# Performance work log

Hardware: AMD Instinct MI355X
Metric: run time of the kernel (lower is better)

The kernel has to match this reference:

```python
import jax, jax.numpy as jnp
import numpy as np

RC = 6.0            # cosine cutoff radius (Angstrom)
N_ANGULAR = 128     # module init arg; output dim = 3*N_ANGULAR
EPS = 1e-12


def cosine_cutoff(d):
    # Behler-style cosine cutoff: 0.5*(cos(pi*d/rc)+1) for d < rc, else 0
    return jnp.where(d < RC, 0.5 * (jnp.cos(jnp.pi * d / RC) + 1.0), 0.0)


def setup_inputs() -> dict:
    key = jax.random.key(0)
    k1, k2, k3, k4 = jax.random.split(key, 4)
    B, N, M = 8, 4096, 96
    L = 20.0  # box length
    positions = jax.random.uniform(k1, (B, N, 3), dtype=jnp.float32) * L
    cell = jnp.tile(jnp.eye(3, dtype=jnp.float32) * L, (B, 1, 1))
    neighbors = jax.random.randint(k2, (B, N, M), 0, N, dtype=jnp.int32)
    offsets = jax.random.randint(k3, (B, N, M, 3), -1, 2).astype(jnp.float32)
    mask = (jax.random.uniform(k4, (B, N, M)) > 0.1).astype(jnp.float32)
    return {"positions": positions, "cell": cell, "offsets": offsets,
            "mask": mask, "neighbors": neighbors}


def reference(positions, cell, offsets, mask, neighbors):
    B, N, M = neighbors.shape
    # gather neighbor positions: pos_j[b,n,m,:] = positions[b, neighbors[b,n,m], :]
    idx = neighbors.reshape(B, N * M)
    pos_j = jnp.take_along_axis(positions, idx[:, :, None], axis=1).reshape(B, N, M, 3)
    # displacement vectors with periodic offsets (offsets in cell coordinates)
    dis_vec = pos_j - positions[:, :, None, :] + jnp.einsum('bnmi,bij->bnmj', offsets, cell)
    distances = jnp.sqrt(jnp.sum(dis_vec * dis_vec, axis=-1) + EPS)  # [B,N,M]
    # cutoff / distance, zeroed where mask == 0
    cut = jnp.where(mask != 0.0, cosine_cutoff(distances) / distances, 0.0)
    # sort neighbors by descending cut value, gather cut-weighted vectors in that order
    order = jnp.argsort(-cut, axis=-1)                       # [B,N,M]
    cut_vec = cut[..., None] * dis_vec                       # [B,N,M,3]
    cut_vec = jnp.take_along_axis(cut_vec, order[..., None], axis=2)
    cut_vec = cut_vec.reshape(B, N, M * 3)
    # scatter into zero-padded descriptor of width 3*n_angular
    f = jnp.zeros((B, N, N_ANGULAR * 3), dtype=positions.dtype)
    f = f.at[:, :, : M * 3].set(cut_vec)
    return f
```

## Files before the change

kernel.cpp:

```cpp
#include <hip/hip_runtime.h>
#include <math.h>

#define M_NB   96
#define OUT_W  384
#define NATOM  4096
#define WPB    16
#define NITER  4

struct Pst {
    int    jA, jB;
    float  mkA, mkB;
    float3 oA, oB;
};

struct Gth {
    float4 pi, pjA, pjB;
};

__device__ __forceinline__ void load_pst(Pst& s,
    const int* __restrict__ nb, const float* __restrict__ mk,
    const float* __restrict__ of, long q, int lane, bool low)
{
    const long eA = q * M_NB + lane;
    s.jA  = nb[eA];
    s.mkA = mk[eA];
    s.oA  = *(const float3*)(of + eA * 3);
    if (low) {
        const long eB = eA + 64;
        s.jB  = nb[eB];
        s.mkB = mk[eB];
        s.oB  = *(const float3*)(of + eB * 3);
    } else {
        s.jB = 0; s.mkB = 0.f; s.oB = make_float3(0.f, 0.f, 0.f);
    }
}

__device__ __forceinline__ void merge3(float4& a4, float2& a2, int base,
                                       float v0, float v1, float v2, int lane)
{
    const int f4lo = 4 * lane;
    const int f2lo = 256 + 2 * lane;
    const float v[3] = {v0, v1, v2};
    #pragma unroll
    for (int t = 0; t < 3; ++t) {
        const int idx = base + t;
        if      (idx == f4lo)     a4.x = v[t];
        else if (idx == f4lo + 1) a4.y = v[t];
        else if (idx == f4lo + 2) a4.z = v[t];
        else if (idx == f4lo + 3) a4.w = v[t];
        else if (idx == f2lo)     a2.x = v[t];
        else if (idx == f2lo + 1) a2.y = v[t];
    }
}

__global__ __launch_bounds__(64 * WPB, 8) void deepmd_angular_kernel(
    const float* __restrict__ positions,
    const float* __restrict__ cell,
    const float* __restrict__ offsets,
    const float* __restrict__ mask,
    const int*   __restrict__ neighbors,
    float*       __restrict__ out,
    int N)
{
    __shared__ float4 pos4_s[NATOM];

    const int tid  = threadIdx.x;
    const int wv   = tid >> 6;
    const int lane = tid & 63;
    const bool low = lane < 32;

    const int p0 = blockIdx.x * (WPB * NITER);
    const int b  = p0 / N;

    {
        const float* pb_ = positions + (size_t)b * N * 3;
        for (int a = tid; a < NATOM; a += 64 * WPB) {
            const float3 v = *(const float3*)(pb_ + 3 * a);
            pos4_s[a] = make_float4(v.x, v.y, v.z, 0.f);
        }
    }
    __syncthreads();

    const float* cb = cell + (size_t)b * 9;
    const float c00 = cb[0], c01 = cb[1], c02 = cb[2];
    const float c10 = cb[3], c11 = cb[4], c12 = cb[5];
    const float c20 = cb[6], c21 = cb[7], c22 = cb[8];

    const long qb = (long)(p0 + wv * NITER);

    Pst s0, s1;
    load_pst(s0, neighbors, mask, offsets, qb + 0, lane, low);
    load_pst(s1, neighbors, mask, offsets, qb + 1, lane, low);
    Gth g0;
    g0.pi  = pos4_s[(int)(qb + 0) - b * N];
    g0.pjA = pos4_s[s0.jA];
    g0.pjB = pos4_s[s0.jB];

    #pragma unroll
    for (int it = 0; it < NITER; ++it) {
        Pst nxs;
        if (it + 2 < NITER)
            load_pst(nxs, neighbors, mask, offsets, qb + it + 2, lane, low);
        Gth g1;
        if (it + 1 < NITER) {
            g1.pi  = pos4_s[(int)(qb + it + 1) - b * N];
            g1.pjA = pos4_s[s1.jA];
            g1.pjB = pos4_s[s1.jB];
        }

        const int q = (int)qb + it;

        const float dxA = g0.pjA.x - g0.pi.x + s0.oA.x * c00 + s0.oA.y * c10 + s0.oA.z * c20;
        const float dyA = g0.pjA.y - g0.pi.y + s0.oA.x * c01 + s0.oA.y * c11 + s0.oA.z * c21;
        const float dzA = g0.pjA.z - g0.pi.z + s0.oA.x * c02 + s0.oA.y * c12 + s0.oA.z * c22;
        const float dA  = sqrtf(dxA * dxA + dyA * dyA + dzA * dzA + 1e-12f);
        float cutA = 0.f;
        if (s0.mkA != 0.f && dA < 6.f)
            cutA = 0.5f * (__cosf(dA * 0.52359877559829887f) + 1.f) / dA;

        float dxB = 0.f, dyB = 0.f, dzB = 0.f, cutB = 0.f;
        if (low) {
            dxB = g0.pjB.x - g0.pi.x + s0.oB.x * c00 + s0.oB.y * c10 + s0.oB.z * c20;
            dyB = g0.pjB.y - g0.pi.y + s0.oB.x * c01 + s0.oB.y * c11 + s0.oB.z * c21;
            dzB = g0.pjB.z - g0.pi.z + s0.oB.x * c02 + s0.oB.y * c12 + s0.oB.z * c22;
            const float dB = sqrtf(dxB * dxB + dyB * dyB + dzB * dzB + 1e-12f);
            if (s0.mkB != 0.f && dB < 6.f)
                cutB = 0.5f * (__cosf(dB * 0.52359877559829887f) + 1.f) / dB;
        }

        const float w0A = cutA * dxA, w1A = cutA * dyA, w2A = cutA * dzA;
        const float w0B = cutB * dxB, w1B = cutB * dyB, w2B = cutB * dzB;

        float4 a4 = make_float4(0.f, 0.f, 0.f, 0.f);
        float2 a2 = make_float2(0.f, 0.f);

        unsigned long long t = __ballot(cutA != 0.f);
        while (t) {
            const int s = (int)__builtin_ctzll(t); t &= t - 1;
            const float c = __shfl(cutA, s);
            const unsigned long long gtA = __ballot(cutA > c);
            const unsigned long long gtB = __ballot(cutB > c);
            const unsigned long long eqA = __ballot(cutA == c);
            const int rank = __popcll(gtA) + __popcll(gtB)
                           + __popcll(eqA & ((1ull << s) - 1ull));
            merge3(a4, a2, 3 * rank,
                   __shfl(w0A, s), __shfl(w1A, s), __shfl(w2A, s), lane);
        }
        t = __ballot(cutB != 0.f);
        while (t) {
            const int s = (int)__builtin_ctzll(t); t &= t - 1;
            const float c = __shfl(cutB, s);
            const unsigned long long gtA = __ballot(cutA > c);
            const unsigned long long gtB = __ballot(cutB > c);
            const unsigned long long eqA = __ballot(cutA == c);
            const unsigned long long eqB = __ballot(cutB == c);
            const int rank = __popcll(gtA) + __popcll(gtB) + __popcll(eqA)
                           + __popcll(eqB & ((1ull << s) - 1ull));
            merge3(a4, a2, 3 * rank,
                   __shfl(w0B, s), __shfl(w1B, s), __shfl(w2B, s), lane);
        }

        float* rowp = out + (size_t)q * OUT_W;
        ((float4*)rowp)[lane] = a4;
        ((float2*)(rowp + 256))[lane] = a2;

        s0 = s1; s1 = nxs; g0 = g1;
    }
}

extern "C" void kernel_launch(void* const* d_in, const int* in_sizes, int n_in,
                              void* d_out, int out_size, void* d_ws, size_t ws_size,
                              hipStream_t stream) {
    const float* positions = (const float*)d_in[0];
    const float* cell      = (const float*)d_in[1];
    const float* offsets   = (const float*)d_in[2];
    const float* mask      = (const float*)d_in[3];
    const int*   neighbors = (const int*)d_in[4];
    float*       out       = (float*)d_out;

    const int BN = in_sizes[0] / 3;
    const int B  = in_sizes[1] / 9;
    const int N  = BN / B;

    dim3 block(64 * WPB, 1, 1);
    dim3 grid(BN / (WPB * NITER), 1, 1);
    deepmd_angular_kernel<<<grid, block, 0, stream>>>(
        positions, cell, offsets, mask, neighbors, out, N);
}
```

Before: 118.3 us.

## Zero output in separate kernel and scatter sorted entries directly to global

```diff
diff --git a/kernel.cpp b/kernel.cpp
--- a/kernel.cpp
+++ b/kernel.cpp
@@ -35,25 +35,17 @@
     }
 }
 
-__device__ __forceinline__ void merge3(float4& a4, float2& a2, int base,
-                                       float v0, float v1, float v2, int lane)
+__global__ __launch_bounds__(256) void fill_zero_kernel(float4* __restrict__ out4,
+                                                        int total4)
 {
-    const int f4lo = 4 * lane;
-    const int f2lo = 256 + 2 * lane;
-    const float v[3] = {v0, v1, v2};
-    #pragma unroll
-    for (int t = 0; t < 3; ++t) {
-        const int idx = base + t;
-        if      (idx == f4lo)     a4.x = v[t];
-        else if (idx == f4lo + 1) a4.y = v[t];
-        else if (idx == f4lo + 2) a4.z = v[t];
-        else if (idx == f4lo + 3) a4.w = v[t];
-        else if (idx == f2lo)     a2.x = v[t];
-        else if (idx == f2lo + 1) a2.y = v[t];
-    }
+    const int stride = gridDim.x * 256;
+    const float4 z4 = make_float4(0.f, 0.f, 0.f, 0.f);
+    #pragma unroll 4
+    for (int i = blockIdx.x * 256 + threadIdx.x; i < total4; i += stride)
+        out4[i] = z4;
 }
 
-__global__ __launch_bounds__(64 * WPB, 8) void deepmd_angular_kernel(
+__global__ __launch_bounds__(64 * WPB, 8) void deepmd_angular_compute(
     const float* __restrict__ positions,
     const float* __restrict__ cell,
     const float* __restrict__ offsets,
@@ -128,11 +120,7 @@
                 cutB = 0.5f * (__cosf(dB * 0.52359877559829887f) + 1.f) / dB;
         }
 
-        const float w0A = cutA * dxA, w1A = cutA * dyA, w2A = cutA * dzA;
-        const float w0B = cutB * dxB, w1B = cutB * dyB, w2B = cutB * dzB;
-
-        float4 a4 = make_float4(0.f, 0.f, 0.f, 0.f);
-        float2 a2 = make_float2(0.f, 0.f);
+        float* rowp = out + (size_t)q * OUT_W;
 
         unsigned long long t = __ballot(cutA != 0.f);
         while (t) {
@@ -143,8 +131,11 @@
             const unsigned long long eqA = __ballot(cutA == c);
             const int rank = __popcll(gtA) + __popcll(gtB)
                            + __popcll(eqA & ((1ull << s) - 1ull));
-            merge3(a4, a2, 3 * rank,
-                   __shfl(w0A, s), __shfl(w1A, s), __shfl(w2A, s), lane);
+            if (lane == s) {
+                rowp[3 * rank + 0] = cutA * dxA;
+                rowp[3 * rank + 1] = cutA * dyA;
+                rowp[3 * rank + 2] = cutA * dzA;
+            }
         }
         t = __ballot(cutB != 0.f);
         while (t) {
@@ -156,13 +147,12 @@
             const unsigned long long eqB = __ballot(cutB == c);
             const int rank = __popcll(gtA) + __popcll(gtB) + __popcll(eqA)
                            + __popcll(eqB & ((1ull << s) - 1ull));
-            merge3(a4, a2, 3 * rank,
-                   __shfl(w0B, s), __shfl(w1B, s), __shfl(w2B, s), lane);
+            if (lane == s) {
+                rowp[3 * rank + 0] = cutB * dxB;
+                rowp[3 * rank + 1] = cutB * dyB;
+                rowp[3 * rank + 2] = cutB * dzB;
+            }
         }
-
-        float* rowp = out + (size_t)q * OUT_W;
-        ((float4*)rowp)[lane] = a4;
-        ((float2*)(rowp + 256))[lane] = a2;
 
         s0 = s1; s1 = nxs; g0 = g1;
     }
@@ -182,8 +172,10 @@
     const int B  = in_sizes[1] / 9;
     const int N  = BN / B;
 
+    fill_zero_kernel<<<2048, 256, 0, stream>>>((float4*)out, out_size / 4);
+
     dim3 block(64 * WPB, 1, 1);
     dim3 grid(BN / (WPB * NITER), 1, 1);
-    deepmd_angular_kernel<<<grid, block, 0, stream>>>(
+    deepmd_angular_compute<<<grid, block, 0, stream>>>(
         positions, cell, offsets, mask, neighbors, out, N);
 }
```

After: 120.9 us. 2.2% more time.
